# Kernel tuning notes

Measured on AMD Instinct MI355X. Metric: run time of the kernel, lower is better.

The kernel has to match this reference:

```python
import jax, jax.numpy as jnp
import numpy as np

N_NODES = 100000
N_EDGES = 800000
D = 128
N_HEADS = 8
D_HEAD = D // N_HEADS


def setup_inputs() -> dict:
    key = jax.random.key(0)
    ks = jax.random.split(key, 8)
    x = jax.random.normal(ks[0], (N_NODES, D), dtype=jnp.float32)
    src = jax.random.randint(ks[1], (N_EDGES,), 0, N_NODES, dtype=jnp.int32)
    dst = jax.random.randint(ks[2], (N_EDGES,), 0, N_NODES, dtype=jnp.int32)
    s = 1.0 / np.sqrt(D)
    # torch nn.Linear convention: y = x @ W.T + b, W ~ U(-1/sqrt(fan_in), ...)
    W_qkv = jax.random.uniform(ks[3], (3 * D, D), jnp.float32, -s, s)
    b_qkv = jax.random.uniform(ks[4], (3 * D,), jnp.float32, -s, s)
    W_out = jax.random.uniform(ks[5], (D, D), jnp.float32, -s, s)
    b_out = jax.random.uniform(ks[6], (D,), jnp.float32, -s, s)
    return {"x": x, "W_qkv": W_qkv, "b_qkv": b_qkv, "W_out": W_out,
            "b_out": b_out, "src": src, "dst": dst}


def reference(x, W_qkv, b_qkv, W_out, b_out, src, dst):
    N = x.shape[0]
    coef = D_HEAD ** -0.5
    qkv = (x @ W_qkv.T + b_qkv).reshape(N, N_HEADS, 3 * D_HEAD)
    q = qkv[..., :D_HEAD]          # [N, H, dh]
    k = qkv[..., D_HEAD:2 * D_HEAD]
    v = qkv[..., 2 * D_HEAD:]
    # u_dot_v: per-edge dot of source k and destination q -> [E, H]
    scores = jnp.einsum('ehd,ehd->eh', k[src], q[dst]) * coef
    # edge_softmax: softmax over edges grouped by destination node
    m = jax.ops.segment_max(scores, dst, num_segments=N)
    m = jnp.where(jnp.isfinite(m), m, 0.0)  # guard zero in-degree nodes
    p = jnp.exp(scores - m[dst])
    denom = jax.ops.segment_sum(p, dst, num_segments=N)
    probs = p / denom[dst]                   # [E, H]
    # u_mul_e_sum: weighted aggregation of source v into destination
    out = jax.ops.segment_sum(v[src] * probs[:, :, None], dst, num_segments=N)
    out = out.reshape(N, D)
    return out @ W_out.T + b_out
```

## Files before the change

### kernel.cpp

```cpp
#include <hip/hip_runtime.h>
#include <hip/hip_bf16.h>

#define N_NODES 100000
#define N_EDGES 800000
#define NB1 98

typedef __attribute__((ext_vector_type(8))) short short8;
typedef __attribute__((ext_vector_type(4))) float f32x4;
typedef __attribute__((ext_vector_type(2))) unsigned int u32x2;

__device__ __forceinline__ float bf2f(ushort u) {
    union { unsigned i; float f; } x; x.i = ((unsigned)u) << 16; return x.f;
}
__device__ __forceinline__ ushort f2bf(float f) {
    union { float f; unsigned u; } x { f };
    unsigned r = x.u + 0x7FFF + ((x.u >> 16) & 1);
    return (ushort)(r >> 16);
}

__global__ __launch_bounds__(128) void prep_all(
    const float* __restrict__ Wq, const float* __restrict__ bq,
    const float* __restrict__ Wo, const float* __restrict__ x,
    const int* __restrict__ dst,
    ushort* __restrict__ Wqb, float* __restrict__ bqp, ushort* __restrict__ Wob,
    ushort* __restrict__ xb, int* __restrict__ counts, int* __restrict__ rank)
{
    int j = blockIdx.x;
    if (j < 384) {
        int h = j / 48, r = j % 48, p;
        if (r < 16)      p = h * 16 + r;
        else if (r < 32) { int d = r - 16; p = 128 + (h * 8 + (d >> 1)) * 4 + (d & 1); }
        else             { int d = r - 32; p = 128 + (h * 8 + (d >> 1)) * 4 + 2 + (d & 1); }
        Wqb[(size_t)p * 128 + threadIdx.x] = f2bf(Wq[(size_t)j * 128 + threadIdx.x]);
        if (threadIdx.x == 0) bqp[p] = bq[j];
    } else if (j < 512) {
        int j2 = j - 384;
        Wob[(size_t)j2 * 128 + threadIdx.x] = f2bf(Wo[(size_t)j2 * 128 + threadIdx.x]);
    } else if (j < 25512) {
        int i = (j - 512) * 128 + threadIdx.x;
        float4 v = reinterpret_cast<const float4*>(x)[i];
        ushort4 o;
        o.x = f2bf(v.x); o.y = f2bf(v.y); o.z = f2bf(v.z); o.w = f2bf(v.w);
        reinterpret_cast<ushort4*>(xb)[i] = o;
    } else {
        int e = (j - 25512) * 128 + threadIdx.x;
        if (e < N_EDGES) rank[e] = atomicAdd(&counts[dst[e]], 1);
    }
}

template<int OUT_BF16>
__global__ __launch_bounds__(256) void gemm_mfma(
    const ushort* __restrict__ A, const ushort* __restrict__ B,
    const float* __restrict__ bias, void* __restrict__ Cv,
    int M, int ldc)
{
    __shared__ ushort As[128][72];
    __shared__ ushort Bs[128][72];
    const int t = threadIdx.x;
    const int lane = t & 63;
    const int w = t >> 6;
    const int wm = w >> 1, wn = w & 1;
    const int n0 = blockIdx.y * 128;
    const int j0 = blockIdx.x * 128;

    f32x4 acc[4][4];
    #pragma unroll
    for (int i = 0; i < 4; ++i)
        #pragma unroll
        for (int j = 0; j < 4; ++j) acc[i][j] = (f32x4){0.f, 0.f, 0.f, 0.f};

    for (int kb = 0; kb < 128; kb += 64) {
        #pragma unroll
        for (int it = 0; it < 4; ++it) {
            int c = it * 256 + t;
            int row = c >> 3, g = c & 7;
            int ar = n0 + row; if (ar >= M) ar = M - 1;
            *reinterpret_cast<short8*>(&As[row][g * 8]) =
                *reinterpret_cast<const short8*>(A + (size_t)ar * 128 + kb + g * 8);
            *reinterpret_cast<short8*>(&Bs[row][g * 8]) =
                *reinterpret_cast<const short8*>(B + (size_t)(j0 + row) * 128 + kb + g * 8);
        }
        __syncthreads();
        #pragma unroll
        for (int kf = 0; kf < 2; ++kf) {
            short8 af[4], bfr[4];
            #pragma unroll
            for (int mf = 0; mf < 4; ++mf)
                af[mf] = *reinterpret_cast<const short8*>(
                    &As[wm * 64 + mf * 16 + (lane & 15)][kf * 32 + (lane >> 4) * 8]);
            #pragma unroll
            for (int nf = 0; nf < 4; ++nf)
                bfr[nf] = *reinterpret_cast<const short8*>(
                    &Bs[wn * 64 + nf * 16 + (lane & 15)][kf * 32 + (lane >> 4) * 8]);
            #pragma unroll
            for (int mf = 0; mf < 4; ++mf)
                #pragma unroll
                for (int nf = 0; nf < 4; ++nf)
                    acc[mf][nf] = __builtin_amdgcn_mfma_f32_16x16x32_bf16(
                        bfr[nf], af[mf], acc[mf][nf], 0, 0, 0);
        }
        __syncthreads();
    }

    const int r = lane & 15, c4 = (lane >> 4) * 4;
    #pragma unroll
    for (int mf = 0; mf < 4; ++mf) {
        int row = n0 + wm * 64 + mf * 16 + r;
        if (row >= M) continue;
        #pragma unroll
        for (int nf = 0; nf < 4; ++nf) {
            int col = j0 + wn * 64 + nf * 16 + c4;
            f32x4 a = acc[mf][nf];
            float v0 = a[0] + bias[col],     v1 = a[1] + bias[col + 1];
            float v2 = a[2] + bias[col + 2], v3 = a[3] + bias[col + 3];
            if (OUT_BF16) {
                u32x2 u;
                u[0] = (unsigned)f2bf(v0) | ((unsigned)f2bf(v1) << 16);
                u[1] = (unsigned)f2bf(v2) | ((unsigned)f2bf(v3) << 16);
                *reinterpret_cast<u32x2*>((ushort*)Cv + (size_t)row * ldc + col) = u;
            } else {
                float4 o = {v0, v1, v2, v3};
                *reinterpret_cast<float4*>((float*)Cv + (size_t)row * ldc + col) = o;
            }
        }
    }
}

__global__ __launch_bounds__(1024) void scan1(
    const int* __restrict__ counts, int* __restrict__ row_start,
    int* __restrict__ bsums)
{
    __shared__ int sd[1024];
    int t = threadIdx.x, i = blockIdx.x * 1024 + t;
    int v = (i < N_NODES) ? counts[i] : 0;
    sd[t] = v; __syncthreads();
    for (int off = 1; off < 1024; off <<= 1) {
        int x = (t >= off) ? sd[t - off] : 0;
        __syncthreads();
        sd[t] += x;
        __syncthreads();
    }
    if (i < N_NODES) row_start[i] = sd[t] - v;
    if (t == 1023) bsums[blockIdx.x] = sd[1023];
}

__global__ __launch_bounds__(256) void scan23(
    const int* __restrict__ bsums, int* __restrict__ row_start)
{
    __shared__ int sd[128];
    __shared__ int se[128];
    const int t = threadIdx.x;
    int v = 0;
    if (t < 128) {
        v = (t < NB1) ? bsums[t] : 0;
        sd[t] = v;
    }
    __syncthreads();
    for (int off = 1; off < 128; off <<= 1) {
        int x = (t < 128 && t >= off) ? sd[t - off] : 0;
        __syncthreads();
        if (t < 128) sd[t] += x;
        __syncthreads();
    }
    if (t < 128) se[t] = sd[t] - v;
    __syncthreads();
    int gid = blockIdx.x * 256 + t;
    if (gid < N_NODES) row_start[gid] += se[gid >> 10];
    if (gid == 0) row_start[N_NODES] = N_EDGES;
}

__global__ __launch_bounds__(256) void fill_csr(
    const int* __restrict__ src, const int* __restrict__ dst,
    const int* __restrict__ rank, const int* __restrict__ row_start,
    int* __restrict__ csr_src)
{
    int e = blockIdx.x * 256 + threadIdx.x;
    if (e >= N_EDGES) return;
    csr_src[row_start[dst[e]] + rank[e]] = src[e];
}

__global__ __launch_bounds__(256) void fused_attn(
    const ushort* __restrict__ qkvp, const int* __restrict__ row_start,
    const int* __restrict__ csr_src, ushort* __restrict__ attnb)
{
    int node = (blockIdx.x * 256 + threadIdx.x) >> 6;
    if (node >= N_NODES) return;
    int lane = threadIdx.x & 63;

    unsigned qb = *reinterpret_cast<const unsigned*>(
        qkvp + (size_t)node * 384 + lane * 2);
    float q0 = bf2f((ushort)qb), q1 = bf2f((ushort)(qb >> 16));

    int beg = row_start[node], end = row_start[node + 1];
    float denom = 0.f, a0 = 0.f, a1 = 0.f;
    const ushort* kvbase = qkvp + 128 + lane * 4;

#define GATHER(s, u) u = *reinterpret_cast<const u32x2*>(kvbase + (size_t)(s) * 384);
#define EDGE(u) { \
        float ps = bf2f((ushort)u[0]) * q0 + bf2f((ushort)(u[0] >> 16)) * q1; \
        ps += __shfl_xor(ps, 1); \
        ps += __shfl_xor(ps, 2); \
        ps += __shfl_xor(ps, 4); \
        float p = __expf(ps * 0.25f); \
        denom += p; \
        a0 += p * bf2f((ushort)u[1]); \
        a1 += p * bf2f((ushort)(u[1] >> 16)); }

    int i = beg;
    for (; i + 4 <= end; i += 4) {
        int s0 = csr_src[i],     s1 = csr_src[i + 1];
        int s2 = csr_src[i + 2], s3 = csr_src[i + 3];
        u32x2 u0, u1, u2, u3;
        GATHER(s0, u0); GATHER(s1, u1); GATHER(s2, u2); GATHER(s3, u3);
        EDGE(u0); EDGE(u1); EDGE(u2); EDGE(u3);
    }
    for (; i < end; ++i) {
        int s = csr_src[i];
        u32x2 u;
        GATHER(s, u);
        EDGE(u);
    }
#undef GATHER
#undef EDGE

    float inv = (end > beg) ? 1.f / denom : 0.f;
    unsigned o = ((unsigned)f2bf(a1 * inv) << 16) | (unsigned)f2bf(a0 * inv);
    *reinterpret_cast<unsigned*>(attnb + (size_t)node * 128 + lane * 2) = o;
}

extern "C" void kernel_launch(void* const* d_in, const int* in_sizes, int n_in,
                              void* d_out, int out_size, void* d_ws, size_t ws_size,
                              hipStream_t stream) {
    const float* x     = (const float*)d_in[0];
    const float* W_qkv = (const float*)d_in[1];
    const float* b_qkv = (const float*)d_in[2];
    const float* W_out = (const float*)d_in[3];
    const float* b_out = (const float*)d_in[4];
    const int*   src   = (const int*)d_in[5];
    const int*   dst   = (const int*)d_in[6];
    float* out = (float*)d_out;

    char* w = (char*)d_ws;
    ushort* qkvp     = (ushort*)(w);
    ushort* attnb    = (ushort*)(w + 76800000);
    ushort* xb       = (ushort*)(w + 102400000);
    ushort* Wqb      = (ushort*)(w + 128000000);
    ushort* Wob      = (ushort*)(w + 128098304);
    float*  bqp      = (float*)(w + 128131072);
    int*    counts   = (int*)(w + 128132608);
    int*    row_start= (int*)(w + 128532608);
    int*    bsums    = (int*)(w + 128932624);
    int*    rank     = (int*)(w + 128933024);
    int*    csr_src  = (int*)(w + 132133024);

    hipMemsetAsync(counts, 0, 400000, stream);

    prep_all<<<31762, 128, 0, stream>>>(W_qkv, b_qkv, W_out, x, dst,
                                        Wqb, bqp, Wob, xb, counts, rank);

    gemm_mfma<1><<<dim3(3, 782), 256, 0, stream>>>(
        xb, Wqb, bqp, (void*)qkvp, N_NODES, 384);

    scan1<<<NB1, 1024, 0, stream>>>(counts, row_start, bsums);
    scan23<<<391, 256, 0, stream>>>(bsums, row_start);
    fill_csr<<<3125, 256, 0, stream>>>(src, dst, rank, row_start, csr_src);

    fused_attn<<<25000, 256, 0, stream>>>(qkvp, row_start, csr_src, attnb);

    gemm_mfma<0><<<dim3(1, 782), 256, 0, stream>>>(
        attnb, Wob, b_out, (void*)out, N_NODES, 128);
}
```

Before: 293.5 us.

## Fuse x bf16 cast into QKV GEMM and store keys as fp8

New measurement: 281.5 us. -4.1%, faster.

```diff
diff --git a/kernel.cpp b/kernel.cpp
--- a/kernel.cpp
+++ b/kernel.cpp
@@ -18,39 +18,33 @@
     return (ushort)(r >> 16);
 }
 
+
 __global__ __launch_bounds__(128) void prep_all(
     const float* __restrict__ Wq, const float* __restrict__ bq,
-    const float* __restrict__ Wo, const float* __restrict__ x,
-    const int* __restrict__ dst,
+    const float* __restrict__ Wo, const int* __restrict__ dst,
     ushort* __restrict__ Wqb, float* __restrict__ bqp, ushort* __restrict__ Wob,
-    ushort* __restrict__ xb, int* __restrict__ counts, int* __restrict__ rank)
+    int* __restrict__ counts, int* __restrict__ rank)
 {
     int j = blockIdx.x;
     if (j < 384) {
         int h = j / 48, r = j % 48, p;
         if (r < 16)      p = h * 16 + r;
-        else if (r < 32) { int d = r - 16; p = 128 + (h * 8 + (d >> 1)) * 4 + (d & 1); }
-        else             { int d = r - 32; p = 128 + (h * 8 + (d >> 1)) * 4 + 2 + (d & 1); }
+        else if (r < 32) p = 128 + h * 16 + (r - 16);
+        else             p = 256 + h * 16 + (r - 32);
         Wqb[(size_t)p * 128 + threadIdx.x] = f2bf(Wq[(size_t)j * 128 + threadIdx.x]);
         if (threadIdx.x == 0) bqp[p] = bq[j];
     } else if (j < 512) {
         int j2 = j - 384;
         Wob[(size_t)j2 * 128 + threadIdx.x] = f2bf(Wo[(size_t)j2 * 128 + threadIdx.x]);
-    } else if (j < 25512) {
-        int i = (j - 512) * 128 + threadIdx.x;
-        float4 v = reinterpret_cast<const float4*>(x)[i];
-        ushort4 o;
-        o.x = f2bf(v.x); o.y = f2bf(v.y); o.z = f2bf(v.z); o.w = f2bf(v.w);
-        reinterpret_cast<ushort4*>(xb)[i] = o;
     } else {
-        int e = (j - 25512) * 128 + threadIdx.x;
+        int e = (j - 512) * 128 + threadIdx.x;
         if (e < N_EDGES) rank[e] = atomicAdd(&counts[dst[e]], 1);
     }
 }
 
-template<int OUT_BF16>
+template<int A_F32, int MODE>
 __global__ __launch_bounds__(256) void gemm_mfma(
-    const ushort* __restrict__ A, const ushort* __restrict__ B,
+    const void* __restrict__ Av, const ushort* __restrict__ B,
     const float* __restrict__ bias, void* __restrict__ Cv,
     int M, int ldc)
 {
@@ -75,8 +69,21 @@
             int c = it * 256 + t;
             int row = c >> 3, g = c & 7;
             int ar = n0 + row; if (ar >= M) ar = M - 1;
-            *reinterpret_cast<short8*>(&As[row][g * 8]) =
-                *reinterpret_cast<const short8*>(A + (size_t)ar * 128 + kb + g * 8);
+            if (A_F32) {
+                const float* ap = (const float*)Av + (size_t)ar * 128 + kb + g * 8;
+                float4 a0 = *reinterpret_cast<const float4*>(ap);
+                float4 a1 = *reinterpret_cast<const float4*>(ap + 4);
+                short8 o;
+                o[0] = (short)f2bf(a0.x); o[1] = (short)f2bf(a0.y);
+                o[2] = (short)f2bf(a0.z); o[3] = (short)f2bf(a0.w);
+                o[4] = (short)f2bf(a1.x); o[5] = (short)f2bf(a1.y);
+                o[6] = (short)f2bf(a1.z); o[7] = (short)f2bf(a1.w);
+                *reinterpret_cast<short8*>(&As[row][g * 8]) = o;
+            } else {
+                *reinterpret_cast<short8*>(&As[row][g * 8]) =
+                    *reinterpret_cast<const short8*>(
+                        (const ushort*)Av + (size_t)ar * 128 + kb + g * 8);
+            }
             *reinterpret_cast<short8*>(&Bs[row][g * 8]) =
                 *reinterpret_cast<const short8*>(B + (size_t)(j0 + row) * 128 + kb + g * 8);
         }
@@ -109,18 +116,27 @@
         if (row >= M) continue;
         #pragma unroll
         for (int nf = 0; nf < 4; ++nf) {
-            int col = j0 + wn * 64 + nf * 16 + c4;
+            int lc = wn * 64 + nf * 16 + c4;
+            int col = j0 + lc;
             f32x4 a = acc[mf][nf];
             float v0 = a[0] + bias[col],     v1 = a[1] + bias[col + 1];
             float v2 = a[2] + bias[col + 2], v3 = a[3] + bias[col + 3];
-            if (OUT_BF16) {
-                u32x2 u;
-                u[0] = (unsigned)f2bf(v0) | ((unsigned)f2bf(v1) << 16);
-                u[1] = (unsigned)f2bf(v2) | ((unsigned)f2bf(v3) << 16);
-                *reinterpret_cast<u32x2*>((ushort*)Cv + (size_t)row * ldc + col) = u;
-            } else {
+            if (MODE == 0) {
                 float4 o = {v0, v1, v2, v3};
                 *reinterpret_cast<float4*>((float*)Cv + (size_t)row * ldc + col) = o;
+            } else {
+                char* rb = (char*)Cv + (size_t)row * 640;
+                if (j0 == 128) {
+                    int pk = __builtin_amdgcn_cvt_pk_fp8_f32(v0, v1, 0, false);
+                    pk     = __builtin_amdgcn_cvt_pk_fp8_f32(v2, v3, pk, true);
+                    *reinterpret_cast<int*>(rb + 256 + lc) = pk;
+                } else {
+                    u32x2 u;
+                    u[0] = (unsigned)f2bf(v0) | ((unsigned)f2bf(v1) << 16);
+                    u[1] = (unsigned)f2bf(v2) | ((unsigned)f2bf(v3) << 16);
+                    int off = (j0 == 0) ? lc * 2 : 384 + lc * 2;
+                    *reinterpret_cast<u32x2*>(rb + off) = u;
+                }
             }
         }
     }
@@ -180,7 +196,7 @@
 }
 
 __global__ __launch_bounds__(256) void fused_attn(
-    const ushort* __restrict__ qkvp, const int* __restrict__ row_start,
+    const char* __restrict__ qkvp, const int* __restrict__ row_start,
     const int* __restrict__ csr_src, ushort* __restrict__ attnb)
 {
     int node = (blockIdx.x * 256 + threadIdx.x) >> 6;
@@ -188,37 +204,44 @@
     int lane = threadIdx.x & 63;
 
     unsigned qb = *reinterpret_cast<const unsigned*>(
-        qkvp + (size_t)node * 384 + lane * 2);
+        qkvp + (size_t)node * 640 + lane * 4);
     float q0 = bf2f((ushort)qb), q1 = bf2f((ushort)(qb >> 16));
 
     int beg = row_start[node], end = row_start[node + 1];
     float denom = 0.f, a0 = 0.f, a1 = 0.f;
-    const ushort* kvbase = qkvp + 128 + lane * 4;
-
-#define GATHER(s, u) u = *reinterpret_cast<const u32x2*>(kvbase + (size_t)(s) * 384);
-#define EDGE(u) { \
-        float ps = bf2f((ushort)u[0]) * q0 + bf2f((ushort)(u[0] >> 16)) * q1; \
-        ps += __shfl_xor(ps, 1); \
-        ps += __shfl_xor(ps, 2); \
-        ps += __shfl_xor(ps, 4); \
-        float p = __expf(ps * 0.25f); \
-        denom += p; \
-        a0 += p * bf2f((ushort)u[1]); \
-        a1 += p * bf2f((ushort)(u[1] >> 16)); }
+    const char* kbase = qkvp + 256 + lane * 2;
+    const char* vbase = qkvp + 384 + lane * 4;
+
+#define GATHER(s, kk, vv) { size_t go_ = (size_t)(s) * 640; \
+        kk = *reinterpret_cast<const ushort*>(kbase + go_); \
+        vv = *reinterpret_cast<const unsigned*>(vbase + go_); }
+#define EDGE(kk, vv) { \
+        float fk0_ = __builtin_amdgcn_cvt_f32_fp8((int)(kk), 0); \
+        float fk1_ = __builtin_amdgcn_cvt_f32_fp8((int)(kk), 1); \
+        float ps_ = fk0_ * q0 + fk1_ * q1; \
+        ps_ += __shfl_xor(ps_, 1); \
+        ps_ += __shfl_xor(ps_, 2); \
+        ps_ += __shfl_xor(ps_, 4); \
+        float p_ = __expf(ps_ * 0.25f); \
+        denom += p_; \
+        a0 += p_ * bf2f((ushort)(vv)); \
+        a1 += p_ * bf2f((ushort)((vv) >> 16)); }
 
     int i = beg;
     for (; i + 4 <= end; i += 4) {
         int s0 = csr_src[i],     s1 = csr_src[i + 1];
         int s2 = csr_src[i + 2], s3 = csr_src[i + 3];
-        u32x2 u0, u1, u2, u3;
-        GATHER(s0, u0); GATHER(s1, u1); GATHER(s2, u2); GATHER(s3, u3);
-        EDGE(u0); EDGE(u1); EDGE(u2); EDGE(u3);
+        ushort k0, k1, k2, k3;
+        unsigned v0, v1, v2, v3;
+        GATHER(s0, k0, v0); GATHER(s1, k1, v1);
+        GATHER(s2, k2, v2); GATHER(s3, k3, v3);
+        EDGE(k0, v0); EDGE(k1, v1); EDGE(k2, v2); EDGE(k3, v3);
     }
     for (; i < end; ++i) {
         int s = csr_src[i];
-        u32x2 u;
-        GATHER(s, u);
-        EDGE(u);
+        ushort kk; unsigned vv;
+        GATHER(s, kk, vv);
+        EDGE(kk, vv);
     }
 #undef GATHER
 #undef EDGE
@@ -241,25 +264,24 @@
     float* out = (float*)d_out;
 
     char* w = (char*)d_ws;
-    ushort* qkvp     = (ushort*)(w);
-    ushort* attnb    = (ushort*)(w + 76800000);
-    ushort* xb       = (ushort*)(w + 102400000);
-    ushort* Wqb      = (ushort*)(w + 128000000);
-    ushort* Wob      = (ushort*)(w + 128098304);
-    float*  bqp      = (float*)(w + 128131072);
-    int*    counts   = (int*)(w + 128132608);
-    int*    row_start= (int*)(w + 128532608);
-    int*    bsums    = (int*)(w + 128932624);
-    int*    rank     = (int*)(w + 128933024);
-    int*    csr_src  = (int*)(w + 132133024);
+    char*   qkvp     = w;
+    ushort* attnb    = (ushort*)(w + 64000000);
+    ushort* Wqb      = (ushort*)(w + 89600000);
+    ushort* Wob      = (ushort*)(w + 89698304);
+    float*  bqp      = (float*)(w + 89731072);
+    int*    counts   = (int*)(w + 89732608);
+    int*    row_start= (int*)(w + 90132608);
+    int*    bsums    = (int*)(w + 90532624);
+    int*    rank     = (int*)(w + 90533024);
+    int*    csr_src  = (int*)(w + 93733024);
 
     hipMemsetAsync(counts, 0, 400000, stream);
 
-    prep_all<<<31762, 128, 0, stream>>>(W_qkv, b_qkv, W_out, x, dst,
-                                        Wqb, bqp, Wob, xb, counts, rank);
-
-    gemm_mfma<1><<<dim3(3, 782), 256, 0, stream>>>(
-        xb, Wqb, bqp, (void*)qkvp, N_NODES, 384);
+    prep_all<<<6762, 128, 0, stream>>>(W_qkv, b_qkv, W_out, dst,
+                                       Wqb, bqp, Wob, counts, rank);
+
+    gemm_mfma<1, 1><<<dim3(3, 782), 256, 0, stream>>>(
+        (const void*)x, Wqb, bqp, (void*)qkvp, N_NODES, 0);
 
     scan1<<<NB1, 1024, 0, stream>>>(counts, row_start, bsums);
     scan23<<<391, 256, 0, stream>>>(bsums, row_start);
@@ -267,6 +289,6 @@
 
     fused_attn<<<25000, 256, 0, stream>>>(qkvp, row_start, csr_src, attnb);
 
-    gemm_mfma<0><<<dim3(1, 782), 256, 0, stream>>>(
-        attnb, Wob, b_out, (void*)out, N_NODES, 128);
-}
+    gemm_mfma<0, 0><<<dim3(1, 782), 256, 0, stream>>>(
+        (const void*)attnb, Wob, b_out, (void*)out, N_NODES, 128);
+}
```
